# Kernel optimization log

Hardware: AMD Instinct MI355X
Metric: run time of the kernel (lower is better)

Reference implementation:

```python
import jax, jax.numpy as jnp
import numpy as np

HIDDEN = 1024
NUM_EXPERTS = 64
MIN_K, MAX_K = 1, 4
THRESHOLD = 0.5
N_TOKENS = 32768


def setup_inputs() -> dict:
    key = jax.random.key(0)
    ks = jax.random.split(key, 6)
    std = 0.02
    h4 = HIDDEN // 4
    return {
        "hidden_states": jax.random.normal(ks[0], (N_TOKENS, HIDDEN), dtype=jnp.float32),
        "router_w": std * jax.random.normal(ks[1], (NUM_EXPERTS, HIDDEN), dtype=jnp.float32),
        "w1": std * jax.random.normal(ks[2], (h4, HIDDEN), dtype=jnp.float32),
        "b1": jnp.zeros((h4,), dtype=jnp.float32),
        "w2": std * jax.random.normal(ks[3], (1, h4), dtype=jnp.float32),
        "b2": jnp.zeros((1,), dtype=jnp.float32),
    }


def reference(hidden_states, router_w, w1, b1, w2, b2):
    # complexity predictor: Linear -> ReLU -> Linear -> Sigmoid, squeeze(-1)
    h = jax.nn.relu(hidden_states @ w1.T + b1)                     # [N, H/4]
    complexity = jax.nn.sigmoid(h @ w2.T + b2)[:, 0]               # [N]
    router_logits = hidden_states @ router_w.T                     # [N, E]

    adaptive_k = jnp.where(complexity > THRESHOLD, MAX_K, MIN_K)   # [N] int

    # vectorized adaptive top-k: take MAX_K everywhere, mask beyond k
    top_vals, top_idx = jax.lax.top_k(router_logits, MAX_K)        # [N, MAX_K]
    pos_mask = jnp.arange(MAX_K)[None, :] < adaptive_k[:, None]    # [N, MAX_K]
    masked_vals = jnp.where(pos_mask, top_vals, -jnp.inf)
    expert_weights = jax.nn.softmax(masked_vals, axis=-1)
    expert_weights = jnp.where(pos_mask, expert_weights, 0.0)      # zeros past k
    selected_experts = jnp.where(pos_mask, top_idx, 0)             # zeros past k

    # routing statistics
    probs = jax.nn.softmax(router_logits, axis=-1)                 # [N, E]
    expert_load = probs.mean(axis=0)                               # [E]
    load_variance = expert_load.var(ddof=1)                        # torch .var() is unbiased
    entropy = -(probs * jnp.log(probs + 1e-8)).sum(axis=-1).mean()

    return router_logits, selected_experts, expert_weights, load_variance, entropy
```

## Files before the change

### kernel.cpp

```cpp
#include <hip/hip_runtime.h>
#include <hip/hip_bf16.h>
#include <math.h>

#define NTOK 32768
#define HID  1024
#define NEXP 64
#define H4   256

typedef __attribute__((ext_vector_type(8))) short bf16x8;
typedef __attribute__((ext_vector_type(4))) float f32x4;

static __device__ __forceinline__ ushort f2bf(float x) {
    unsigned u = __float_as_uint(x);
    unsigned r = (u + 0x7FFFu + ((u >> 16) & 1u)) >> 16;
    return (ushort)r;
}

static __device__ __forceinline__ void split3r(float x, ushort &h, ushort &m, ushort &l) {
    h = f2bf(x);
    const float r1 = x - __uint_as_float(((unsigned)h) << 16);
    m = f2bf(r1);
    const float r2 = r1 - __uint_as_float(((unsigned)m) << 16);
    l = f2bf(r2);
}

#define SWZ(row, us) ((us) ^ (((row) & 7) << 3))

__global__ __launch_bounds__(256) void prep_kernel(
    const float* __restrict__ W1, const float* __restrict__ RW,
    ushort* __restrict__ W1f, ushort* __restrict__ RWf)
{
    if (blockIdx.x < 256) {
        const int id = blockIdx.x * 256 + threadIdx.x;
        const int c  = id >> 8;
        const int k0 = (id & 255) * 4;
        const float4 v = *(const float4*)(W1 + (size_t)c * HID + k0);
        const int p = k0 >> 5, quad = (k0 >> 3) & 3, kk = k0 & 7;
        const int cg = c >> 6, j = (c >> 4) & 3, l15 = c & 15;
        const int lane = quad * 16 + l15;
        const size_t base = (size_t)p * 16384 + cg * 4096 + j * 1024 + lane * 8 + kk;
        const float xs[4] = {v.x, v.y, v.z, v.w};
        ushort hv[4], lv[4];
#pragma unroll
        for (int q = 0; q < 4; q++) {
            const ushort h = f2bf(xs[q]);
            hv[q] = h;
            lv[q] = f2bf(xs[q] - __uint_as_float(((unsigned)h) << 16));
        }
        *(ushort4*)(W1f + base)       = make_ushort4(hv[0], hv[1], hv[2], hv[3]);
        *(ushort4*)(W1f + base + 512) = make_ushort4(lv[0], lv[1], lv[2], lv[3]);
    } else {
        const int e  = blockIdx.x - 256;
        const int k0 = threadIdx.x * 4;
        const float4 v = *(const float4*)(RW + (size_t)e * HID + k0);
        const int p = k0 >> 5, quad = (k0 >> 3) & 3, kk = k0 & 7;
        const int cg = e >> 4, l15 = e & 15;
        const int lane = quad * 16 + l15;
        const size_t base = (size_t)p * 6144 + cg * 1536 + lane * 8 + kk;
        const float xs[4] = {v.x, v.y, v.z, v.w};
        ushort h[4], m[4], l[4];
#pragma unroll
        for (int q = 0; q < 4; q++) split3r(xs[q], h[q], m[q], l[q]);
        *(ushort4*)(RWf + base)        = make_ushort4(h[0], h[1], h[2], h[3]);
        *(ushort4*)(RWf + base + 512)  = make_ushort4(m[0], m[1], m[2], m[3]);
        *(ushort4*)(RWf + base + 1024) = make_ushort4(l[0], l[1], l[2], l[3]);
    }
}

__global__ __launch_bounds__(512, 4) void fused_mfma(
    const float* __restrict__ X,
    const ushort* __restrict__ RWf, const ushort* __restrict__ W1f,
    const float* __restrict__ B1, const float* __restrict__ W2,
    float* __restrict__ logits, float* __restrict__ s2ws)
{
    __shared__ __align__(16) ushort Xh[2][2048], Xm[2][2048], Xl[2][2048];
    __shared__ float red[4][64];

    const int tid  = threadIdx.x;
    const int lane = tid & 63;
    const int w    = tid >> 6;
    const int quad = lane >> 4, l15 = lane & 15;
    const int tok0 = blockIdx.x * 64;
    const int rp   = w >> 2;
    const int cg   = w & 3;

    const int xrow = tid >> 3;
    const int xoff = (tid & 7) * 4;

    f32x4 accL[2];
    f32x4 accP[2][4];
#pragma unroll
    for (int f = 0; f < 2; f++) {
        accL[f] = (f32x4){0.f, 0.f, 0.f, 0.f};
#pragma unroll
        for (int j = 0; j < 4; j++) accP[f][j] = (f32x4){0.f, 0.f, 0.f, 0.f};
    }

    const float* __restrict__ xsrc = X + (size_t)(tok0 + xrow) * HID + xoff;
    const ushort* __restrict__ rwbase = RWf + (size_t)cg * 1536 + lane * 8;
    const ushort* __restrict__ w1base = W1f + (size_t)cg * 4096 + lane * 8;

    {
        const float4 x0 = *(const float4*)(xsrc);
        const float xs[4] = {x0.x, x0.y, x0.z, x0.w};
        ushort hv[4], mv[4], lv[4];
#pragma unroll
        for (int q = 0; q < 4; q++) split3r(xs[q], hv[q], mv[q], lv[q]);
        const int us = SWZ(xrow, xrow * 32 + xoff);
        *(ushort4*)&Xh[0][us] = make_ushort4(hv[0], hv[1], hv[2], hv[3]);
        *(ushort4*)&Xm[0][us] = make_ushort4(mv[0], mv[1], mv[2], mv[3]);
        *(ushort4*)&Xl[0][us] = make_ushort4(lv[0], lv[1], lv[2], lv[3]);
    }
    __syncthreads();

    for (int p = 0; p < 32; ++p) {
        const int cur = p & 1;

        const ushort* __restrict__ rwp = rwbase + (size_t)p * 6144;
        const bf16x8 rbh = *(const bf16x8*)(rwp);
        const bf16x8 rbm = *(const bf16x8*)(rwp + 512);
        const bf16x8 rbl = *(const bf16x8*)(rwp + 1024);
        const ushort* __restrict__ w1p = w1base + (size_t)p * 16384;
        bf16x8 bwh[4], bwl[4];
#pragma unroll
        for (int j = 0; j < 4; ++j) {
            bwh[j] = *(const bf16x8*)(w1p + j * 1024);
            bwl[j] = *(const bf16x8*)(w1p + j * 1024 + 512);
        }

        const float4 xv = *(const float4*)(xsrc + ((p + 1) & 31) * 32);

        bf16x8 axh[2], axm[2], axl[2];
#pragma unroll
        for (int f = 0; f < 2; ++f) {
            const int ra = rp * 32 + f * 16 + l15;
            const int ua = SWZ(ra, ra * 32 + quad * 8);
            axh[f] = *(const bf16x8*)&Xh[cur][ua];
            axm[f] = *(const bf16x8*)&Xm[cur][ua];
            axl[f] = *(const bf16x8*)&Xl[cur][ua];
        }

        {
            const float xs[4] = {xv.x, xv.y, xv.z, xv.w};
            ushort hv[4], mv[4], lv[4];
#pragma unroll
            for (int q = 0; q < 4; q++) split3r(xs[q], hv[q], mv[q], lv[q]);
            const int us = SWZ(xrow, xrow * 32 + xoff);
            *(ushort4*)&Xh[cur ^ 1][us] = make_ushort4(hv[0], hv[1], hv[2], hv[3]);
            *(ushort4*)&Xm[cur ^ 1][us] = make_ushort4(mv[0], mv[1], mv[2], mv[3]);
            *(ushort4*)&Xl[cur ^ 1][us] = make_ushort4(lv[0], lv[1], lv[2], lv[3]);
        }

#pragma unroll
        for (int f = 0; f < 2; ++f) {
            accL[f] = __builtin_amdgcn_mfma_f32_16x16x32_bf16(axh[f], rbh, accL[f], 0, 0, 0);
            accL[f] = __builtin_amdgcn_mfma_f32_16x16x32_bf16(axm[f], rbh, accL[f], 0, 0, 0);
            accL[f] = __builtin_amdgcn_mfma_f32_16x16x32_bf16(axh[f], rbm, accL[f], 0, 0, 0);
            accL[f] = __builtin_amdgcn_mfma_f32_16x16x32_bf16(axl[f], rbh, accL[f], 0, 0, 0);
            accL[f] = __builtin_amdgcn_mfma_f32_16x16x32_bf16(axh[f], rbl, accL[f], 0, 0, 0);
            accL[f] = __builtin_amdgcn_mfma_f32_16x16x32_bf16(axm[f], rbm, accL[f], 0, 0, 0);
        }

#pragma unroll
        for (int j = 0; j < 4; ++j)
#pragma unroll
            for (int f = 0; f < 2; ++f) {
                accP[f][j] = __builtin_amdgcn_mfma_f32_16x16x32_bf16(axh[f], bwh[j], accP[f][j], 0, 0, 0);
                accP[f][j] = __builtin_amdgcn_mfma_f32_16x16x32_bf16(axm[f], bwh[j], accP[f][j], 0, 0, 0);
                accP[f][j] = __builtin_amdgcn_mfma_f32_16x16x32_bf16(axh[f], bwl[j], accP[f][j], 0, 0, 0);
            }

        __syncthreads();
    }

#pragma unroll
    for (int f = 0; f < 2; ++f)
#pragma unroll
        for (int r = 0; r < 4; ++r)
            logits[(size_t)(tok0 + (rp * 2 + f) * 16 + quad * 4 + r) * NEXP
                   + cg * 16 + l15] = accL[f][r];

    float w2r[4], b1r[4];
#pragma unroll
    for (int j = 0; j < 4; ++j) {
        const int col = (cg * 4 + j) * 16 + l15;
        w2r[j] = W2[col];
        b1r[j] = B1[col];
    }
#pragma unroll
    for (int f = 0; f < 2; ++f) {
#pragma unroll
        for (int r = 0; r < 4; ++r) {
            float s = 0.f;
#pragma unroll
            for (int j = 0; j < 4; ++j) {
                const float hval = accP[f][j][r] + b1r[j];
                s = fmaf(w2r[j], fmaxf(hval, 0.f), s);
            }
            s += __shfl_xor(s, 1);
            s += __shfl_xor(s, 2);
            s += __shfl_xor(s, 4);
            s += __shfl_xor(s, 8);
            if (l15 == 0)
                red[cg][rp * 32 + f * 16 + quad * 4 + r] = s;
        }
    }
    __syncthreads();
    if (tid < 64)
        s2ws[tok0 + tid] = red[0][tid] + red[1][tid] + red[2][tid] + red[3][tid];
}

__global__ __launch_bounds__(64) void route_kernel(
    const float* __restrict__ logits, const float* __restrict__ s2ws,
    const float* __restrict__ B2, float* __restrict__ sel,
    float* __restrict__ wts, float* __restrict__ load_sum,
    float* __restrict__ ent_sum)
{
    const int lane = threadIdx.x;
    const int tok  = blockIdx.x * 64 + lane;

    float r[64];
    const float* lr = logits + (size_t)tok * NEXP;
#pragma unroll
    for (int e4 = 0; e4 < 16; e4++) {
        float4 v = *(const float4*)(lr + e4 * 4);
        r[e4 * 4 + 0] = v.x; r[e4 * 4 + 1] = v.y;
        r[e4 * 4 + 2] = v.z; r[e4 * 4 + 3] = v.w;
    }

    float v0 = -1e30f, v1 = -1e30f, v2 = -1e30f, v3 = -1e30f;
    int   i0 = 0, i1 = 0, i2 = 0, i3 = 0;
#pragma unroll
    for (int e = 0; e < 64; e++) {
        const float v = r[e];
        if (v > v3) {
            if (v > v2) {
                if (v > v1) {
                    if (v > v0) { v3=v2;i3=i2; v2=v1;i2=i1; v1=v0;i1=i0; v0=v;i0=e; }
                    else        { v3=v2;i3=i2; v2=v1;i2=i1; v1=v;i1=e; }
                } else          { v3=v2;i3=i2; v2=v;i2=e; }
            } else              { v3=v;i3=e; }
        }
    }

    const float s2 = s2ws[tok] + B2[0];
    const bool k4 = (s2 > 0.f);

    float w0, w1v, w2v, w3v;
    int   s1i, s2i, s3i;
    if (k4) {
        const float e0 = expf(v0 - v0), e1 = expf(v1 - v0);
        const float e2 = expf(v2 - v0), e3 = expf(v3 - v0);
        const float inv4 = 1.f / (e0 + e1 + e2 + e3);
        w0 = e0 * inv4; w1v = e1 * inv4; w2v = e2 * inv4; w3v = e3 * inv4;
        s1i = i1; s2i = i2; s3i = i3;
    } else {
        w0 = 1.f; w1v = 0.f; w2v = 0.f; w3v = 0.f;
        s1i = 0; s2i = 0; s3i = 0;
    }
    {
        float4 sv = {(float)i0, (float)s1i, (float)s2i, (float)s3i};
        float4 wv = {w0, w1v, w2v, w3v};
        *(float4*)(sel + (size_t)tok * 4) = sv;
        *(float4*)(wts + (size_t)tok * 4) = wv;
    }

    const float mx = v0;
    float S = 0.f, pz = 0.f;
#pragma unroll
    for (int e = 0; e < 64; e++) {
        const float z = r[e] - mx;
        const float t = expf(z);
        S += t; pz = fmaf(t, z, pz);
        r[e] = t;
    }
    const float inv = 1.f / S;
    float ent = logf(S) - pz * inv;

    float myload = 0.f;
#pragma unroll
    for (int e = 0; e < 64; e++) {
        float s = r[e] * inv;
        s += __shfl_xor(s, 1);
        s += __shfl_xor(s, 2);
        s += __shfl_xor(s, 4);
        s += __shfl_xor(s, 8);
        s += __shfl_xor(s, 16);
        s += __shfl_xor(s, 32);
        if (lane == e) myload = s;
    }
    atomicAdd(&load_sum[lane], myload);

    ent += __shfl_xor(ent, 1);
    ent += __shfl_xor(ent, 2);
    ent += __shfl_xor(ent, 4);
    ent += __shfl_xor(ent, 8);
    ent += __shfl_xor(ent, 16);
    ent += __shfl_xor(ent, 32);
    if (lane == 0) atomicAdd(ent_sum, ent);
}

__global__ void finalize_kernel(const float* __restrict__ load_sum,
                                const float* __restrict__ ent_sum,
                                float* __restrict__ out_scal)
{
    const int lane = threadIdx.x;
    const float le = load_sum[lane] * (1.f / (float)NTOK);
    float s = le;
#pragma unroll
    for (int o = 32; o >= 1; o >>= 1) s += __shfl_xor(s, o);
    const float mean = s * (1.f / 64.f);
    const float d = le - mean;
    float v = d * d;
#pragma unroll
    for (int o = 32; o >= 1; o >>= 1) v += __shfl_xor(v, o);
    if (lane == 0) {
        out_scal[0] = v * (1.f / 63.f);
        out_scal[1] = ent_sum[0] * (1.f / (float)NTOK);
    }
}

extern "C" void kernel_launch(void* const* d_in, const int* in_sizes, int n_in,
                              void* d_out, int out_size, void* d_ws, size_t ws_size,
                              hipStream_t stream) {
    const float* X  = (const float*)d_in[0];
    const float* RW = (const float*)d_in[1];
    const float* W1 = (const float*)d_in[2];
    const float* B1 = (const float*)d_in[3];
    const float* W2 = (const float*)d_in[4];
    const float* B2 = (const float*)d_in[5];

    float* out    = (float*)d_out;
    float* logits = out;
    float* sel    = out + (size_t)NTOK * NEXP;
    float* wts    = sel + (size_t)NTOK * 4;
    float* scal   = wts + (size_t)NTOK * 4;

    float* s2ws     = (float*)d_ws;
    float* load_sum = s2ws + NTOK;
    float* ent_sum  = load_sum + 64;
    ushort* W1f = (ushort*)(s2ws + NTOK + 256);
    ushort* RWf = W1f + (size_t)32 * 16384;

    hipMemsetAsync(load_sum, 0, 65 * sizeof(float), stream);

    prep_kernel<<<320, 256, 0, stream>>>(W1, RW, W1f, RWf);
    fused_mfma<<<NTOK / 64, 512, 0, stream>>>(X, RWf, W1f, B1, W2, logits, s2ws);
    route_kernel<<<NTOK / 64, 64, 0, stream>>>(logits, s2ws, B2, sel, wts, load_sum, ent_sum);
    finalize_kernel<<<1, 64, 0, stream>>>(load_sum, ent_sum, scal);
}
```

Baseline: 298.6 us.

## Double token tile per block and software-pipeline weight and X prefetch

The fused MFMA kernel now handles 128 tokens per block instead of 64. Each wave computes four 16-row fragments, so every loaded weight fragment is reused across twice as many tokens. The K loop is unrolled by two with a templated step. Router weights are prefetched one step ahead and X two steps ahead into registers, and a raw barrier with sched_barrier replaces __syncthreads. In exchange, register pressure and LDS use rise, launch bounds drop to two blocks per CU, and half as many blocks are launched.

Result: faster. 280.2 us (-6.2%).

```diff
diff --git a/kernel.cpp b/kernel.cpp
--- a/kernel.cpp
+++ b/kernel.cpp
@@ -8,6 +8,7 @@
 #define H4   256
 
 typedef __attribute__((ext_vector_type(8))) short bf16x8;
+typedef __attribute__((ext_vector_type(8))) unsigned short u16x8;
 typedef __attribute__((ext_vector_type(4))) float f32x4;
 
 static __device__ __forceinline__ ushort f2bf(float x) {
@@ -67,117 +68,154 @@
     }
 }
 
-__global__ __launch_bounds__(512, 4) void fused_mfma(
+template<int PH>
+__device__ __forceinline__ void kstep(
+    int p, int rp, int cg, int lane, int quad, int l15, int row, int kc,
+    const float* __restrict__ xsrc,
+    const ushort* __restrict__ RWf, const ushort* __restrict__ W1f,
+    ushort (&Xh)[2][4096], ushort (&Xm)[2][4096], ushort (&Xl)[2][4096],
+    bf16x8 (&rwh)[2], bf16x8 (&rwm)[2], bf16x8 (&rwl)[2],
+    float4 (&xp)[2][2],
+    f32x4 (&accL)[4], f32x4 (&accP)[4][4])
+{
+    const ushort* __restrict__ w1p = W1f + (size_t)p * 16384 + cg * 4096 + lane * 8;
+    bf16x8 bwh[4], bwl[4];
+#pragma unroll
+    for (int j = 0; j < 4; ++j) {
+        bwh[j] = *(const bf16x8*)(w1p + j * 1024);
+        bwl[j] = *(const bf16x8*)(w1p + j * 1024 + 512);
+    }
+    {
+        const ushort* __restrict__ rwp =
+            RWf + (size_t)((p + 1) & 31) * 6144 + cg * 1536 + lane * 8;
+        rwh[PH ^ 1] = *(const bf16x8*)(rwp);
+        rwm[PH ^ 1] = *(const bf16x8*)(rwp + 512);
+        rwl[PH ^ 1] = *(const bf16x8*)(rwp + 1024);
+    }
+    xp[PH ^ 1][0] = *(const float4*)(xsrc + (size_t)((p + 2) & 31) * 32);
+    xp[PH ^ 1][1] = *(const float4*)(xsrc + (size_t)((p + 2) & 31) * 32 + 4);
+
+    bf16x8 axh[4], axm[4], axl[4];
+#pragma unroll
+    for (int f = 0; f < 4; ++f) {
+        const int ra = rp * 64 + f * 16 + l15;
+        const int ua = SWZ(ra, ra * 32 + quad * 8);
+        axh[f] = *(const bf16x8*)&Xh[PH][ua];
+        axm[f] = *(const bf16x8*)&Xm[PH][ua];
+        axl[f] = *(const bf16x8*)&Xl[PH][ua];
+    }
+
+    {
+        const float xs[8] = {xp[PH][0].x, xp[PH][0].y, xp[PH][0].z, xp[PH][0].w,
+                             xp[PH][1].x, xp[PH][1].y, xp[PH][1].z, xp[PH][1].w};
+        u16x8 sh, sm, sl;
+#pragma unroll
+        for (int q = 0; q < 8; ++q) {
+            ushort h, m, l;
+            split3r(xs[q], h, m, l);
+            sh[q] = h; sm[q] = m; sl[q] = l;
+        }
+        const int us = SWZ(row, row * 32 + kc * 8);
+        *(u16x8*)&Xh[PH ^ 1][us] = sh;
+        *(u16x8*)&Xm[PH ^ 1][us] = sm;
+        *(u16x8*)&Xl[PH ^ 1][us] = sl;
+    }
+
+#pragma unroll
+    for (int f = 0; f < 4; ++f) {
+        accL[f] = __builtin_amdgcn_mfma_f32_16x16x32_bf16(axh[f], rwh[PH], accL[f], 0, 0, 0);
+        accL[f] = __builtin_amdgcn_mfma_f32_16x16x32_bf16(axm[f], rwh[PH], accL[f], 0, 0, 0);
+        accL[f] = __builtin_amdgcn_mfma_f32_16x16x32_bf16(axh[f], rwm[PH], accL[f], 0, 0, 0);
+        accL[f] = __builtin_amdgcn_mfma_f32_16x16x32_bf16(axl[f], rwh[PH], accL[f], 0, 0, 0);
+        accL[f] = __builtin_amdgcn_mfma_f32_16x16x32_bf16(axh[f], rwl[PH], accL[f], 0, 0, 0);
+        accL[f] = __builtin_amdgcn_mfma_f32_16x16x32_bf16(axm[f], rwm[PH], accL[f], 0, 0, 0);
+    }
+#pragma unroll
+    for (int j = 0; j < 4; ++j)
+#pragma unroll
+        for (int f = 0; f < 4; ++f) {
+            accP[f][j] = __builtin_amdgcn_mfma_f32_16x16x32_bf16(axh[f], bwh[j], accP[f][j], 0, 0, 0);
+            accP[f][j] = __builtin_amdgcn_mfma_f32_16x16x32_bf16(axm[f], bwh[j], accP[f][j], 0, 0, 0);
+            accP[f][j] = __builtin_amdgcn_mfma_f32_16x16x32_bf16(axh[f], bwl[j], accP[f][j], 0, 0, 0);
+        }
+
+    asm volatile("s_waitcnt lgkmcnt(0)" ::: "memory");
+    __builtin_amdgcn_s_barrier();
+    __builtin_amdgcn_sched_barrier(0);
+}
+
+__global__ __launch_bounds__(512, 2) void fused_mfma(
     const float* __restrict__ X,
     const ushort* __restrict__ RWf, const ushort* __restrict__ W1f,
     const float* __restrict__ B1, const float* __restrict__ W2,
     float* __restrict__ logits, float* __restrict__ s2ws)
 {
-    __shared__ __align__(16) ushort Xh[2][2048], Xm[2][2048], Xl[2][2048];
-    __shared__ float red[4][64];
+    __shared__ __align__(16) ushort Xh[2][4096], Xm[2][4096], Xl[2][4096];
+    __shared__ float red[4][128];
 
     const int tid  = threadIdx.x;
     const int lane = tid & 63;
     const int w    = tid >> 6;
     const int quad = lane >> 4, l15 = lane & 15;
-    const int tok0 = blockIdx.x * 64;
+    const int tok0 = blockIdx.x * 128;
     const int rp   = w >> 2;
     const int cg   = w & 3;
 
-    const int xrow = tid >> 3;
-    const int xoff = (tid & 7) * 4;
-
-    f32x4 accL[2];
-    f32x4 accP[2][4];
-#pragma unroll
-    for (int f = 0; f < 2; f++) {
+    const int row = tid >> 2;
+    const int kc  = tid & 3;
+
+    f32x4 accL[4];
+    f32x4 accP[4][4];
+#pragma unroll
+    for (int f = 0; f < 4; f++) {
         accL[f] = (f32x4){0.f, 0.f, 0.f, 0.f};
 #pragma unroll
         for (int j = 0; j < 4; j++) accP[f][j] = (f32x4){0.f, 0.f, 0.f, 0.f};
     }
 
-    const float* __restrict__ xsrc = X + (size_t)(tok0 + xrow) * HID + xoff;
-    const ushort* __restrict__ rwbase = RWf + (size_t)cg * 1536 + lane * 8;
-    const ushort* __restrict__ w1base = W1f + (size_t)cg * 4096 + lane * 8;
-
-    {
-        const float4 x0 = *(const float4*)(xsrc);
-        const float xs[4] = {x0.x, x0.y, x0.z, x0.w};
-        ushort hv[4], mv[4], lv[4];
-#pragma unroll
-        for (int q = 0; q < 4; q++) split3r(xs[q], hv[q], mv[q], lv[q]);
-        const int us = SWZ(xrow, xrow * 32 + xoff);
-        *(ushort4*)&Xh[0][us] = make_ushort4(hv[0], hv[1], hv[2], hv[3]);
-        *(ushort4*)&Xm[0][us] = make_ushort4(mv[0], mv[1], mv[2], mv[3]);
-        *(ushort4*)&Xl[0][us] = make_ushort4(lv[0], lv[1], lv[2], lv[3]);
-    }
+    const float* __restrict__ xsrc = X + (size_t)(tok0 + row) * HID + kc * 8;
+
+    bf16x8 rwh[2], rwm[2], rwl[2];
+    float4 xp[2][2];
+
+    {
+        const float4 a0 = *(const float4*)(xsrc);
+        const float4 a1 = *(const float4*)(xsrc + 4);
+        const float xs[8] = {a0.x, a0.y, a0.z, a0.w, a1.x, a1.y, a1.z, a1.w};
+        u16x8 sh, sm, sl;
+#pragma unroll
+        for (int q = 0; q < 8; ++q) {
+            ushort h, m, l;
+            split3r(xs[q], h, m, l);
+            sh[q] = h; sm[q] = m; sl[q] = l;
+        }
+        const int us = SWZ(row, row * 32 + kc * 8);
+        *(u16x8*)&Xh[0][us] = sh;
+        *(u16x8*)&Xm[0][us] = sm;
+        *(u16x8*)&Xl[0][us] = sl;
+    }
+    {
+        const ushort* __restrict__ rwp = RWf + (size_t)cg * 1536 + lane * 8;
+        rwh[0] = *(const bf16x8*)(rwp);
+        rwm[0] = *(const bf16x8*)(rwp + 512);
+        rwl[0] = *(const bf16x8*)(rwp + 1024);
+    }
+    xp[0][0] = *(const float4*)(xsrc + 32);
+    xp[0][1] = *(const float4*)(xsrc + 36);
     __syncthreads();
 
-    for (int p = 0; p < 32; ++p) {
-        const int cur = p & 1;
-
-        const ushort* __restrict__ rwp = rwbase + (size_t)p * 6144;
-        const bf16x8 rbh = *(const bf16x8*)(rwp);
-        const bf16x8 rbm = *(const bf16x8*)(rwp + 512);
-        const bf16x8 rbl = *(const bf16x8*)(rwp + 1024);
-        const ushort* __restrict__ w1p = w1base + (size_t)p * 16384;
-        bf16x8 bwh[4], bwl[4];
-#pragma unroll
-        for (int j = 0; j < 4; ++j) {
-            bwh[j] = *(const bf16x8*)(w1p + j * 1024);
-            bwl[j] = *(const bf16x8*)(w1p + j * 1024 + 512);
-        }
-
-        const float4 xv = *(const float4*)(xsrc + ((p + 1) & 31) * 32);
-
-        bf16x8 axh[2], axm[2], axl[2];
-#pragma unroll
-        for (int f = 0; f < 2; ++f) {
-            const int ra = rp * 32 + f * 16 + l15;
-            const int ua = SWZ(ra, ra * 32 + quad * 8);
-            axh[f] = *(const bf16x8*)&Xh[cur][ua];
-            axm[f] = *(const bf16x8*)&Xm[cur][ua];
-            axl[f] = *(const bf16x8*)&Xl[cur][ua];
-        }
-
-        {
-            const float xs[4] = {xv.x, xv.y, xv.z, xv.w};
-            ushort hv[4], mv[4], lv[4];
-#pragma unroll
-            for (int q = 0; q < 4; q++) split3r(xs[q], hv[q], mv[q], lv[q]);
-            const int us = SWZ(xrow, xrow * 32 + xoff);
-            *(ushort4*)&Xh[cur ^ 1][us] = make_ushort4(hv[0], hv[1], hv[2], hv[3]);
-            *(ushort4*)&Xm[cur ^ 1][us] = make_ushort4(mv[0], mv[1], mv[2], mv[3]);
-            *(ushort4*)&Xl[cur ^ 1][us] = make_ushort4(lv[0], lv[1], lv[2], lv[3]);
-        }
-
-#pragma unroll
-        for (int f = 0; f < 2; ++f) {
-            accL[f] = __builtin_amdgcn_mfma_f32_16x16x32_bf16(axh[f], rbh, accL[f], 0, 0, 0);
-            accL[f] = __builtin_amdgcn_mfma_f32_16x16x32_bf16(axm[f], rbh, accL[f], 0, 0, 0);
-            accL[f] = __builtin_amdgcn_mfma_f32_16x16x32_bf16(axh[f], rbm, accL[f], 0, 0, 0);
-            accL[f] = __builtin_amdgcn_mfma_f32_16x16x32_bf16(axl[f], rbh, accL[f], 0, 0, 0);
-            accL[f] = __builtin_amdgcn_mfma_f32_16x16x32_bf16(axh[f], rbl, accL[f], 0, 0, 0);
-            accL[f] = __builtin_amdgcn_mfma_f32_16x16x32_bf16(axm[f], rbm, accL[f], 0, 0, 0);
-        }
-
-#pragma unroll
-        for (int j = 0; j < 4; ++j)
-#pragma unroll
-            for (int f = 0; f < 2; ++f) {
-                accP[f][j] = __builtin_amdgcn_mfma_f32_16x16x32_bf16(axh[f], bwh[j], accP[f][j], 0, 0, 0);
-                accP[f][j] = __builtin_amdgcn_mfma_f32_16x16x32_bf16(axm[f], bwh[j], accP[f][j], 0, 0, 0);
-                accP[f][j] = __builtin_amdgcn_mfma_f32_16x16x32_bf16(axh[f], bwl[j], accP[f][j], 0, 0, 0);
-            }
-
-        __syncthreads();
-    }
-
-#pragma unroll
-    for (int f = 0; f < 2; ++f)
+    for (int p = 0; p < 32; p += 2) {
+        kstep<0>(p,     rp, cg, lane, quad, l15, row, kc, xsrc, RWf, W1f,
+                 Xh, Xm, Xl, rwh, rwm, rwl, xp, accL, accP);
+        kstep<1>(p + 1, rp, cg, lane, quad, l15, row, kc, xsrc, RWf, W1f,
+                 Xh, Xm, Xl, rwh, rwm, rwl, xp, accL, accP);
+    }
+
+#pragma unroll
+    for (int f = 0; f < 4; ++f)
 #pragma unroll
         for (int r = 0; r < 4; ++r)
-            logits[(size_t)(tok0 + (rp * 2 + f) * 16 + quad * 4 + r) * NEXP
+            logits[(size_t)(tok0 + rp * 64 + f * 16 + quad * 4 + r) * NEXP
                    + cg * 16 + l15] = accL[f][r];
 
     float w2r[4], b1r[4];
@@ -188,7 +226,7 @@
         b1r[j] = B1[col];
     }
 #pragma unroll
-    for (int f = 0; f < 2; ++f) {
+    for (int f = 0; f < 4; ++f) {
 #pragma unroll
         for (int r = 0; r < 4; ++r) {
             float s = 0.f;
@@ -202,11 +240,11 @@
             s += __shfl_xor(s, 4);
             s += __shfl_xor(s, 8);
             if (l15 == 0)
-                red[cg][rp * 32 + f * 16 + quad * 4 + r] = s;
+                red[cg][rp * 64 + f * 16 + quad * 4 + r] = s;
         }
     }
     __syncthreads();
-    if (tid < 64)
+    if (tid < 128)
         s2ws[tok0 + tid] = red[0][tid] + red[1][tid] + red[2][tid] + red[3][tid];
 }
 
@@ -345,7 +383,7 @@
     hipMemsetAsync(load_sum, 0, 65 * sizeof(float), stream);
 
     prep_kernel<<<320, 256, 0, stream>>>(W1, RW, W1f, RWf);
-    fused_mfma<<<NTOK / 64, 512, 0, stream>>>(X, RWf, W1f, B1, W2, logits, s2ws);
+    fused_mfma<<<NTOK / 128, 512, 0, stream>>>(X, RWf, W1f, B1, W2, logits, s2ws);
     route_kernel<<<NTOK / 64, 64, 0, stream>>>(logits, s2ws, B2, sel, wts, load_sum, ent_sum);
     finalize_kernel<<<1, 64, 0, stream>>>(load_sum, ent_sum, scal);
 }
```
